# Optimization experiments

Measured on AMD Instinct MI355X. Metric: run time of the kernel, lower is better.

Reference implementation:

```python
import jax, jax.numpy as jnp
import numpy as np

N_NODES = 50000
N_FEAT = 128
N_HIDDEN = 256
N_CLASSES = 1
N_EDGES = 800000


def gcn_layer(x, src, dst, W, b, n_nodes):
    """GCNConv: D^-1/2 (A + I) D^-1/2 X W + b, via gather-scatter over edges."""
    h = x @ W  # [N, out]
    # add self loops
    loop = jnp.arange(n_nodes, dtype=src.dtype)
    s = jnp.concatenate([src, loop])
    d = jnp.concatenate([dst, loop])
    deg = jax.ops.segment_sum(jnp.ones_like(d, dtype=h.dtype), d, num_segments=n_nodes)
    inv_sqrt = jax.lax.rsqrt(jnp.maximum(deg, 1.0))
    norm = inv_sqrt[s] * inv_sqrt[d]  # [E+N]
    msgs = h[s] * norm[:, None]       # gather: [E+N, out]
    out = jax.ops.segment_sum(msgs, d, num_segments=n_nodes)  # scatter-add
    return out + b


def setup_inputs() -> dict:
    key = jax.random.key(0)
    k1, k2, k3, k4 = jax.random.split(key, 4)
    x = jax.random.normal(k1, (N_NODES, N_FEAT), dtype=jnp.float32)
    edge_index = jax.random.randint(k2, (2, N_EDGES), 0, N_NODES, dtype=jnp.int32)
    s1 = 1.0 / np.sqrt(N_FEAT)
    s2 = 1.0 / np.sqrt(N_HIDDEN)
    W1 = jax.random.uniform(k3, (N_FEAT, N_HIDDEN), jnp.float32, -s1, s1)
    b1 = jnp.zeros((N_HIDDEN,), jnp.float32)
    W2 = jax.random.uniform(k4, (N_HIDDEN, N_CLASSES), jnp.float32, -s2, s2)
    b2 = jnp.zeros((N_CLASSES,), jnp.float32)
    return {"x": x, "edge_index": edge_index, "W1": W1, "b1": b1, "W2": W2, "b2": b2}


def reference(x, edge_index, W1, b1, W2, b2):
    src, dst = edge_index[0], edge_index[1]
    n = x.shape[0]
    h = gcn_layer(x, src, dst, W1, b1, n)
    h = jax.nn.relu(h)  # dropout=0.0 -> identity
    out = gcn_layer(h, src, dst, W2, b2, n)
    return out  # [N, n_classes]
```

## Files before the change

kernel.cpp:

```cpp
#include <hip/hip_runtime.h>

typedef unsigned int uint;
typedef unsigned short ushort;
typedef __attribute__((ext_vector_type(8))) short short8;
typedef __attribute__((ext_vector_type(4))) float f32x4;

#define CAP   64
#define BM16  16
#define STR   68
#define NPB   192
#define NBIN  261
#define CAPB  4096
#define EPB   4096

__device__ __forceinline__ float bf_lo(uint p) { return __uint_as_float(p << 16); }
__device__ __forceinline__ float bf_hi(uint p) { return __uint_as_float(p & 0xffff0000u); }
__device__ __forceinline__ uint rne_lo(uint u) { return (u + 0x7fffu + ((u >> 16) & 1u)) >> 16; }
__device__ __forceinline__ uint rne_hi(uint u) { return (u + 0x7fffu + ((u >> 16) & 1u)) & 0xffff0000u; }

__global__ __launch_bounds__(1024) void k_part(
    const int* __restrict__ src, const int* __restrict__ dst,
    int* __restrict__ binCnt, uint* __restrict__ binData,
    const float* __restrict__ W1, uint* __restrict__ wpack, int E, int nblk_e) {
  int t = threadIdx.x;
  if ((int)blockIdx.x >= nblk_e) {
    int g = ((int)blockIdx.x - nblk_e) * 256 + (t & 255);
    if ((t >> 8) == 0 && g < 4096) {
      int kk = g >> 10, rem = g & 1023, ntile = rem >> 6, ln = rem & 63;
      int quad = ln >> 4, nn = ntile * 16 + (ln & 15);
      uint d[4];
#pragma unroll
      for (int jp = 0; jp < 4; ++jp) {
        int k = kk * 32 + quad * 8 + 2 * jp;
        uint lov = rne_lo(__float_as_uint(W1[k * 256 + nn]));
        uint hiv = rne_hi(__float_as_uint(W1[(k + 1) * 256 + nn]));
        d[jp] = lov | hiv;
      }
      *(uint4*)&wpack[g * 4] = make_uint4(d[0], d[1], d[2], d[3]);
    }
    return;
  }
  __shared__ int hist[NBIN];
  __shared__ int base[NBIN];
  for (int i = t; i < NBIN; i += 1024) hist[i] = 0;
  __syncthreads();
  int s[4], d[4], b[4];
  bool v[4];
#pragma unroll
  for (int j = 0; j < 4; ++j) {
    int e = blockIdx.x * EPB + j * 1024 + t;
    v[j] = e < E;
    if (v[j]) {
      s[j] = src[e];
      d[j] = dst[e];
      b[j] = d[j] / NPB;
      atomicAdd(&hist[b[j]], 1);
    }
  }
  __syncthreads();
  for (int i = t; i < NBIN; i += 1024) {
    int h = hist[i];
    base[i] = h ? atomicAdd(&binCnt[i], h) : 0;
    hist[i] = 0;
  }
  __syncthreads();
#pragma unroll
  for (int j = 0; j < 4; ++j) {
    if (v[j]) {
      int r = atomicAdd(&hist[b[j]], 1);
      int idx = base[b[j]] + r;
      if (idx < CAPB)
        binData[b[j] * CAPB + idx] = (uint)s[j] | ((uint)d[j] << 16);
    }
  }
}

__global__ __launch_bounds__(1024) void k_bucketize(
    const uint* __restrict__ binData, const int* __restrict__ binCnt,
    ushort* __restrict__ col, int* __restrict__ cnt,
    const float2* __restrict__ x2, uint* __restrict__ xs, float* __restrict__ inv,
    int N) {
  __shared__ ushort col_l[NPB * CAP];
  __shared__ int cnt_l[NPB];
  int b = blockIdx.x, t = threadIdx.x;
  int lo = b * NPB;
  for (int i = t; i < NPB; i += 1024) cnt_l[i] = 0;
  __syncthreads();
  int m = min(binCnt[b], CAPB);
  const uint* bd = &binData[b * CAPB];
  for (int e = t; e < m; e += 1024) {
    uint pr = bd[e];
    int sv = pr & 0xffffu;
    int dl = (int)(pr >> 16) - lo;
    int p = atomicAdd(&cnt_l[dl], 1);
    if (p < CAP) col_l[dl * CAP + p] = (ushort)sv;
  }
  __syncthreads();
  int nh = min(NPB, N - lo);
  if (nh <= 0) return;
  for (int i = t; i < nh; i += 1024) {
    int c = cnt_l[i];
    cnt[lo + i] = c;
    inv[lo + i] = rsqrtf((float)(c + 1));
  }
  uint* cg = (uint*)(col + (size_t)lo * CAP);
  const uint* cl = (const uint*)col_l;
  int nu = nh * (CAP / 2);
  for (int i = t; i < nu; i += 1024) cg[i] = cl[i];
  int nc = nh * 64;
  for (int i = t; i < nc; i += 1024) {
    int node = lo + (i >> 6);
    float invd = rsqrtf((float)(cnt_l[i >> 6] + 1));
    float2 f = x2[(size_t)node * 64 + (i & 63)];
    xs[(size_t)node * 64 + (i & 63)] =
        rne_lo(__float_as_uint(invd * f.x)) | rne_hi(__float_as_uint(invd * f.y));
  }
}

__global__ __launch_bounds__(256, 2) void k_agg_gemm(
    const uint* __restrict__ xs, const ushort* __restrict__ col,
    const int* __restrict__ cnt, const float* __restrict__ inv,
    const uint* __restrict__ wpack, const float* __restrict__ b1,
    const float* __restrict__ W2, float* __restrict__ cz, int N) {
  __shared__ uint As[BM16 * STR];
  __shared__ float red[64];
  int t = threadIdx.x, wave = t >> 6, lane = t & 63;
  int m0 = blockIdx.x * BM16;

  for (int rr = 0; rr < 4; ++rr) {
    int m = wave * 4 + rr;
    int node = m0 + m;
    float2 acc = make_float2(0.f, 0.f);
    if (node < N) {
      uint pd = xs[(size_t)node * 64 + lane];
      acc.x = bf_lo(pd);
      acc.y = bf_hi(pd);
      int e = min(cnt[node], CAP);
      int ce = (int)col[node * CAP + lane];
      int p = 0;
      for (; p + 15 < e; p += 16) {
        uint pv[16];
#pragma unroll
        for (int j = 0; j < 16; ++j) {
          int s = __shfl(ce, p + j);
          pv[j] = xs[(size_t)s * 64 + lane];
        }
#pragma unroll
        for (int j = 0; j < 16; ++j) { acc.x += bf_lo(pv[j]); acc.y += bf_hi(pv[j]); }
      }
      for (; p + 3 < e; p += 4) {
        uint pv[4];
#pragma unroll
        for (int j = 0; j < 4; ++j) {
          int s = __shfl(ce, p + j);
          pv[j] = xs[(size_t)s * 64 + lane];
        }
#pragma unroll
        for (int j = 0; j < 4; ++j) { acc.x += bf_lo(pv[j]); acc.y += bf_hi(pv[j]); }
      }
      for (; p < e; ++p) {
        int s = __shfl(ce, p);
        uint p0 = xs[(size_t)s * 64 + lane];
        acc.x += bf_lo(p0); acc.y += bf_hi(p0);
      }
      float invd = inv[node];
      acc.x *= invd;
      acc.y *= invd;
    }
    As[m * STR + lane] = rne_lo(__float_as_uint(acc.x)) | rne_hi(__float_as_uint(acc.y));
  }
  __syncthreads();

  int quad = lane >> 4, mrow = lane & 15;
  f32x4 acc[4];
#pragma unroll
  for (int nt = 0; nt < 4; ++nt) acc[nt] = (f32x4){0.f, 0.f, 0.f, 0.f};
#pragma unroll
  for (int kk = 0; kk < 4; ++kk) {
    short8 af = *(const short8*)&As[mrow * STR + kk * 16 + quad * 4];
#pragma unroll
    for (int nt = 0; nt < 4; ++nt) {
      int ntile = wave * 4 + nt;
      short8 bf = *(const short8*)&wpack[((kk * 16 + ntile) * 64 + lane) * 4];
      acc[nt] = __builtin_amdgcn_mfma_f32_16x16x32_bf16(af, bf, acc[nt], 0, 0, 0);
    }
  }

  float partial[4] = {0.f, 0.f, 0.f, 0.f};
#pragma unroll
  for (int nt = 0; nt < 4; ++nt) {
    int c = (wave * 4 + nt) * 16 + mrow;
    float b1c = b1[c], w2c = W2[c];
#pragma unroll
    for (int r = 0; r < 4; ++r) {
      float h = fmaxf(acc[nt][r] + b1c, 0.f);
      partial[r] = fmaf(h, w2c, partial[r]);
    }
  }
#pragma unroll
  for (int r = 0; r < 4; ++r) {
    float p = partial[r];
    p += __shfl_xor(p, 1); p += __shfl_xor(p, 2);
    p += __shfl_xor(p, 4); p += __shfl_xor(p, 8);
    if (mrow == 0) red[wave * 16 + quad * 4 + r] = p;
  }
  __syncthreads();
  if (t < 16) {
    int node = m0 + t;
    if (node < N) {
      float s = red[t] + red[16 + t] + red[32 + t] + red[48 + t];
      cz[node] = inv[node] * s;
    }
  }
}

__global__ void k_agg2(const ushort* __restrict__ col, const int* __restrict__ cnt,
                       const float* __restrict__ inv, const float* __restrict__ cz,
                       const float* __restrict__ b2, float* __restrict__ out, int N) {
  int g = blockIdx.x * blockDim.x + threadIdx.x;
  int node = g >> 2, q = g & 3;
  if (node >= N) return;
  int e = min(cnt[node], CAP);
  float acc = (q == 0) ? cz[node] : 0.f;
  const ushort* cp = &col[node * CAP];
  for (int p = q; p < e; p += 4) acc += cz[cp[p]];
  acc += __shfl_xor(acc, 1);
  acc += __shfl_xor(acc, 2);
  if (q == 0) out[node] = inv[node] * acc + b2[0];
}

extern "C" void kernel_launch(void* const* d_in, const int* in_sizes, int n_in,
                              void* d_out, int out_size, void* d_ws, size_t ws_size,
                              hipStream_t stream) {
  const float2* x2 = (const float2*)d_in[0];
  const int*    ei = (const int*)d_in[1];
  const float*  W1 = (const float*)d_in[2];
  const float*  b1 = (const float*)d_in[3];
  const float*  W2 = (const float*)d_in[4];
  const float*  b2 = (const float*)d_in[5];
  int N = in_sizes[0] / 128;
  int E = in_sizes[1] / 2;
  const int* src = ei;
  const int* dst = ei + E;
  float* out = (float*)d_out;

  char* w = (char*)d_ws;
  size_t o = 0;
  auto carve = [&](size_t bytes) { char* p = w + o; o += (bytes + 255) & ~(size_t)255; return p; };
  int*    binCnt  = (int*)   carve((size_t)NBIN * 4);
  int*    cnt     = (int*)   carve((size_t)N * 4);
  uint*   binData = (uint*)  carve((size_t)NBIN * CAPB * 4);
  ushort* col     = (ushort*)carve((size_t)N * CAP * 2);
  uint*   xs      = (uint*)  carve((size_t)N * 64 * 4);
  float*  inv     = (float*) carve((size_t)N * 4);
  uint*   wpack   = (uint*)  carve(16384 * 4);
  float*  cz      = (float*) carve((size_t)N * 4);

  hipMemsetAsync(binCnt, 0, (size_t)NBIN * sizeof(int), stream);

  int nblk_e = (E + EPB - 1) / EPB;
  k_part<<<nblk_e + 16, 1024, 0, stream>>>(src, dst, binCnt, binData, W1, wpack, E, nblk_e);

  k_bucketize<<<NBIN, 1024, 0, stream>>>(binData, binCnt, col, cnt, x2, xs, inv, N);

  k_agg_gemm<<<(N + BM16 - 1) / BM16, 256, 0, stream>>>(
      xs, col, cnt, inv, wpack, b1, W2, cz, N);

  long long tot2 = (long long)N * 4;
  k_agg2<<<(int)((tot2 + 255) / 256), 256, 0, stream>>>(col, cnt, inv, cz, b2, out, N);
}
```

Baseline: 147.3 us.

## Move bf16 conversion of x into partition kernel and apply source norms in aggregation

The fp32-to-bf16 conversion of node features moves out of the bucketize kernel and into extra blocks of the partition kernel, so it no longer waits on degree counts. Because the converted features are now unscaled, the aggregation kernel applies each source's 1/sqrt(deg) weight per edge via a shuffled coefficient and an FMA, and scales the self term by the node's own norm. This shortens the serial bucketize stage and overlaps the conversion with edge partitioning. The cost is a random read of cnt per neighbor, one rsqrt and one extra shuffle per edge in the gather loop, and slightly different bf16 rounding because scaling now happens after quantization.

```diff
diff --git a/kernel.cpp b/kernel.cpp
--- a/kernel.cpp
+++ b/kernel.cpp
@@ -12,6 +12,8 @@
 #define NBIN  261
 #define CAPB  4096
 #define EPB   4096
+#define NB_W  16
+#define NB_X  112
 
 __device__ __forceinline__ float bf_lo(uint p) { return __uint_as_float(p << 16); }
 __device__ __forceinline__ float bf_hi(uint p) { return __uint_as_float(p & 0xffff0000u); }
@@ -21,22 +23,33 @@
 __global__ __launch_bounds__(1024) void k_part(
     const int* __restrict__ src, const int* __restrict__ dst,
     int* __restrict__ binCnt, uint* __restrict__ binData,
-    const float* __restrict__ W1, uint* __restrict__ wpack, int E, int nblk_e) {
+    const float* __restrict__ W1, uint* __restrict__ wpack,
+    const float2* __restrict__ x2, uint* __restrict__ xs,
+    int E, int nconv, int nblk_e) {
   int t = threadIdx.x;
-  if ((int)blockIdx.x >= nblk_e) {
-    int g = ((int)blockIdx.x - nblk_e) * 256 + (t & 255);
-    if ((t >> 8) == 0 && g < 4096) {
-      int kk = g >> 10, rem = g & 1023, ntile = rem >> 6, ln = rem & 63;
-      int quad = ln >> 4, nn = ntile * 16 + (ln & 15);
-      uint d[4];
-#pragma unroll
-      for (int jp = 0; jp < 4; ++jp) {
-        int k = kk * 32 + quad * 8 + 2 * jp;
-        uint lov = rne_lo(__float_as_uint(W1[k * 256 + nn]));
-        uint hiv = rne_hi(__float_as_uint(W1[(k + 1) * 256 + nn]));
-        d[jp] = lov | hiv;
-      }
-      *(uint4*)&wpack[g * 4] = make_uint4(d[0], d[1], d[2], d[3]);
+  int bx = (int)blockIdx.x;
+  if (bx >= nblk_e) {
+    int role = bx - nblk_e;
+    if (role < NB_W) {
+      int g = role * 256 + (t & 255);
+      if ((t >> 8) == 0) {
+        int kk = g >> 10, rem = g & 1023, ntile = rem >> 6, ln = rem & 63;
+        int quad = ln >> 4, nn = ntile * 16 + (ln & 15);
+        uint d[4];
+#pragma unroll
+        for (int jp = 0; jp < 4; ++jp) {
+          int k = kk * 32 + quad * 8 + 2 * jp;
+          uint lov = rne_lo(__float_as_uint(W1[k * 256 + nn]));
+          uint hiv = rne_hi(__float_as_uint(W1[(k + 1) * 256 + nn]));
+          d[jp] = lov | hiv;
+        }
+        *(uint4*)&wpack[g * 4] = make_uint4(d[0], d[1], d[2], d[3]);
+      }
+    } else {
+      for (int g = (role - NB_W) * 1024 + t; g < nconv; g += NB_X * 1024) {
+        float2 f = x2[g];
+        xs[g] = rne_lo(__float_as_uint(f.x)) | rne_hi(__float_as_uint(f.y));
+      }
     }
     return;
   }
@@ -48,7 +61,7 @@
   bool v[4];
 #pragma unroll
   for (int j = 0; j < 4; ++j) {
-    int e = blockIdx.x * EPB + j * 1024 + t;
+    int e = bx * EPB + j * 1024 + t;
     v[j] = e < E;
     if (v[j]) {
       s[j] = src[e];
@@ -77,9 +90,7 @@
 
 __global__ __launch_bounds__(1024) void k_bucketize(
     const uint* __restrict__ binData, const int* __restrict__ binCnt,
-    ushort* __restrict__ col, int* __restrict__ cnt,
-    const float2* __restrict__ x2, uint* __restrict__ xs, float* __restrict__ inv,
-    int N) {
+    ushort* __restrict__ col, int* __restrict__ cnt, float* __restrict__ inv, int N) {
   __shared__ ushort col_l[NPB * CAP];
   __shared__ int cnt_l[NPB];
   int b = blockIdx.x, t = threadIdx.x;
@@ -107,14 +118,6 @@
   const uint* cl = (const uint*)col_l;
   int nu = nh * (CAP / 2);
   for (int i = t; i < nu; i += 1024) cg[i] = cl[i];
-  int nc = nh * 64;
-  for (int i = t; i < nc; i += 1024) {
-    int node = lo + (i >> 6);
-    float invd = rsqrtf((float)(cnt_l[i >> 6] + 1));
-    float2 f = x2[(size_t)node * 64 + (i & 63)];
-    xs[(size_t)node * 64 + (i & 63)] =
-        rne_lo(__float_as_uint(invd * f.x)) | rne_hi(__float_as_uint(invd * f.y));
-  }
 }
 
 __global__ __launch_bounds__(256, 2) void k_agg_gemm(
@@ -132,38 +135,49 @@
     int node = m0 + m;
     float2 acc = make_float2(0.f, 0.f);
     if (node < N) {
+      float invd = inv[node];
       uint pd = xs[(size_t)node * 64 + lane];
-      acc.x = bf_lo(pd);
-      acc.y = bf_hi(pd);
+      acc.x = invd * bf_lo(pd);
+      acc.y = invd * bf_hi(pd);
       int e = min(cnt[node], CAP);
       int ce = (int)col[node * CAP + lane];
+      float cw = rsqrtf((float)(cnt[ce] + 1));
       int p = 0;
       for (; p + 15 < e; p += 16) {
-        uint pv[16];
+        uint pv[16]; float cv[16];
 #pragma unroll
         for (int j = 0; j < 16; ++j) {
           int s = __shfl(ce, p + j);
+          cv[j] = __shfl(cw, p + j);
           pv[j] = xs[(size_t)s * 64 + lane];
         }
 #pragma unroll
-        for (int j = 0; j < 16; ++j) { acc.x += bf_lo(pv[j]); acc.y += bf_hi(pv[j]); }
+        for (int j = 0; j < 16; ++j) {
+          acc.x = fmaf(bf_lo(pv[j]), cv[j], acc.x);
+          acc.y = fmaf(bf_hi(pv[j]), cv[j], acc.y);
+        }
       }
       for (; p + 3 < e; p += 4) {
-        uint pv[4];
+        uint pv[4]; float cv[4];
 #pragma unroll
         for (int j = 0; j < 4; ++j) {
           int s = __shfl(ce, p + j);
+          cv[j] = __shfl(cw, p + j);
           pv[j] = xs[(size_t)s * 64 + lane];
         }
 #pragma unroll
-        for (int j = 0; j < 4; ++j) { acc.x += bf_lo(pv[j]); acc.y += bf_hi(pv[j]); }
+        for (int j = 0; j < 4; ++j) {
+          acc.x = fmaf(bf_lo(pv[j]), cv[j], acc.x);
+          acc.y = fmaf(bf_hi(pv[j]), cv[j], acc.y);
+        }
       }
       for (; p < e; ++p) {
         int s = __shfl(ce, p);
+        float c = __shfl(cw, p);
         uint p0 = xs[(size_t)s * 64 + lane];
-        acc.x += bf_lo(p0); acc.y += bf_hi(p0);
-      }
-      float invd = inv[node];
+        acc.x = fmaf(bf_lo(p0), c, acc.x);
+        acc.y = fmaf(bf_hi(p0), c, acc.y);
+      }
       acc.x *= invd;
       acc.y *= invd;
     }
@@ -258,10 +272,12 @@
 
   hipMemsetAsync(binCnt, 0, (size_t)NBIN * sizeof(int), stream);
 
+  int nconv = N * 64;
   int nblk_e = (E + EPB - 1) / EPB;
-  k_part<<<nblk_e + 16, 1024, 0, stream>>>(src, dst, binCnt, binData, W1, wpack, E, nblk_e);
-
-  k_bucketize<<<NBIN, 1024, 0, stream>>>(binData, binCnt, col, cnt, x2, xs, inv, N);
+  k_part<<<nblk_e + NB_W + NB_X, 1024, 0, stream>>>(
+      src, dst, binCnt, binData, W1, wpack, x2, xs, E, nconv, nblk_e);
+
+  k_bucketize<<<NBIN, 1024, 0, stream>>>(binData, binCnt, col, cnt, inv, N);
 
   k_agg_gemm<<<(N + BM16 - 1) / BM16, 256, 0, stream>>>(
       xs, col, cnt, inv, wpack, b1, W2, cz, N);
```

After: 149.8 us. Within noise of the previous version (+1.7%).

## Split x conversion into separate kernel and prefetch per-row metadata in aggregation

Applied to the files above, without the earlier changes.

Moves the scaling and bf16 packing of x out of the 261-block bucketize kernel into a new fully parallel elementwise kernel, so the conversion is no longer limited to a few large blocks. The aggregation kernel now loads count, column list, self feature and inverse degree for all four rows up front, so their latencies overlap. The cost is one extra launch and more registers held live in the aggregation kernel.

```diff
diff --git a/kernel.cpp b/kernel.cpp
--- a/kernel.cpp
+++ b/kernel.cpp
@@ -12,6 +12,7 @@
 #define NBIN  261
 #define CAPB  4096
 #define EPB   4096
+#define NB_W  16
 
 __device__ __forceinline__ float bf_lo(uint p) { return __uint_as_float(p << 16); }
 __device__ __forceinline__ float bf_hi(uint p) { return __uint_as_float(p & 0xffff0000u); }
@@ -23,9 +24,10 @@
     int* __restrict__ binCnt, uint* __restrict__ binData,
     const float* __restrict__ W1, uint* __restrict__ wpack, int E, int nblk_e) {
   int t = threadIdx.x;
-  if ((int)blockIdx.x >= nblk_e) {
-    int g = ((int)blockIdx.x - nblk_e) * 256 + (t & 255);
-    if ((t >> 8) == 0 && g < 4096) {
+  int bx = (int)blockIdx.x;
+  if (bx >= nblk_e) {
+    int g = (bx - nblk_e) * 256 + (t & 255);
+    if ((t >> 8) == 0) {
       int kk = g >> 10, rem = g & 1023, ntile = rem >> 6, ln = rem & 63;
       int quad = ln >> 4, nn = ntile * 16 + (ln & 15);
       uint d[4];
@@ -48,7 +50,7 @@
   bool v[4];
 #pragma unroll
   for (int j = 0; j < 4; ++j) {
-    int e = blockIdx.x * EPB + j * 1024 + t;
+    int e = bx * EPB + j * 1024 + t;
     v[j] = e < E;
     if (v[j]) {
       s[j] = src[e];
@@ -77,9 +79,7 @@
 
 __global__ __launch_bounds__(1024) void k_bucketize(
     const uint* __restrict__ binData, const int* __restrict__ binCnt,
-    ushort* __restrict__ col, int* __restrict__ cnt,
-    const float2* __restrict__ x2, uint* __restrict__ xs, float* __restrict__ inv,
-    int N) {
+    ushort* __restrict__ col, int* __restrict__ cnt, float* __restrict__ inv, int N) {
   __shared__ ushort col_l[NPB * CAP];
   __shared__ int cnt_l[NPB];
   int b = blockIdx.x, t = threadIdx.x;
@@ -107,13 +107,15 @@
   const uint* cl = (const uint*)col_l;
   int nu = nh * (CAP / 2);
   for (int i = t; i < nu; i += 1024) cg[i] = cl[i];
-  int nc = nh * 64;
-  for (int i = t; i < nc; i += 1024) {
-    int node = lo + (i >> 6);
-    float invd = rsqrtf((float)(cnt_l[i >> 6] + 1));
-    float2 f = x2[(size_t)node * 64 + (i & 63)];
-    xs[(size_t)node * 64 + (i & 63)] =
-        rne_lo(__float_as_uint(invd * f.x)) | rne_hi(__float_as_uint(invd * f.y));
+}
+
+__global__ void k_prep2(const float2* __restrict__ x2, const float* __restrict__ inv,
+                        uint* __restrict__ xs, int nconv) {
+  int gid = blockIdx.x * blockDim.x + threadIdx.x;
+  if (gid < nconv) {
+    float invd = inv[gid >> 6];
+    float2 f = x2[gid];
+    xs[gid] = rne_lo(__float_as_uint(invd * f.x)) | rne_hi(__float_as_uint(invd * f.y));
   }
 }
 
@@ -127,46 +129,51 @@
   int t = threadIdx.x, wave = t >> 6, lane = t & 63;
   int m0 = blockIdx.x * BM16;
 
+  int eA[4]; int ceA[4]; uint pdA[4]; float invA[4];
+#pragma unroll
+  for (int rr = 0; rr < 4; ++rr) {
+    int node = m0 + wave * 4 + rr;
+    bool ok = node < N;
+    int nc = ok ? node : 0;
+    eA[rr]   = ok ? min(cnt[nc], CAP) : 0;
+    ceA[rr]  = (int)col[(size_t)nc * CAP + lane];
+    pdA[rr]  = ok ? xs[(size_t)nc * 64 + lane] : 0u;
+    invA[rr] = ok ? inv[nc] : 0.f;
+  }
+
   for (int rr = 0; rr < 4; ++rr) {
     int m = wave * 4 + rr;
-    int node = m0 + m;
-    float2 acc = make_float2(0.f, 0.f);
-    if (node < N) {
-      uint pd = xs[(size_t)node * 64 + lane];
-      acc.x = bf_lo(pd);
-      acc.y = bf_hi(pd);
-      int e = min(cnt[node], CAP);
-      int ce = (int)col[node * CAP + lane];
-      int p = 0;
-      for (; p + 15 < e; p += 16) {
-        uint pv[16];
-#pragma unroll
-        for (int j = 0; j < 16; ++j) {
-          int s = __shfl(ce, p + j);
-          pv[j] = xs[(size_t)s * 64 + lane];
-        }
-#pragma unroll
-        for (int j = 0; j < 16; ++j) { acc.x += bf_lo(pv[j]); acc.y += bf_hi(pv[j]); }
+    float2 acc = make_float2(bf_lo(pdA[rr]), bf_hi(pdA[rr]));
+    int e = eA[rr];
+    int ce = ceA[rr];
+    int p = 0;
+    for (; p + 15 < e; p += 16) {
+      uint pv[16];
+#pragma unroll
+      for (int j = 0; j < 16; ++j) {
+        int s = __shfl(ce, p + j);
+        pv[j] = xs[(size_t)s * 64 + lane];
       }
-      for (; p + 3 < e; p += 4) {
-        uint pv[4];
-#pragma unroll
-        for (int j = 0; j < 4; ++j) {
-          int s = __shfl(ce, p + j);
-          pv[j] = xs[(size_t)s * 64 + lane];
-        }
-#pragma unroll
-        for (int j = 0; j < 4; ++j) { acc.x += bf_lo(pv[j]); acc.y += bf_hi(pv[j]); }
+#pragma unroll
+      for (int j = 0; j < 16; ++j) { acc.x += bf_lo(pv[j]); acc.y += bf_hi(pv[j]); }
+    }
+    for (; p + 3 < e; p += 4) {
+      uint pv[4];
+#pragma unroll
+      for (int j = 0; j < 4; ++j) {
+        int s = __shfl(ce, p + j);
+        pv[j] = xs[(size_t)s * 64 + lane];
       }
-      for (; p < e; ++p) {
-        int s = __shfl(ce, p);
-        uint p0 = xs[(size_t)s * 64 + lane];
-        acc.x += bf_lo(p0); acc.y += bf_hi(p0);
-      }
-      float invd = inv[node];
-      acc.x *= invd;
-      acc.y *= invd;
-    }
+#pragma unroll
+      for (int j = 0; j < 4; ++j) { acc.x += bf_lo(pv[j]); acc.y += bf_hi(pv[j]); }
+    }
+    for (; p < e; ++p) {
+      int s = __shfl(ce, p);
+      uint p0 = xs[(size_t)s * 64 + lane];
+      acc.x += bf_lo(p0); acc.y += bf_hi(p0);
+    }
+    acc.x *= invA[rr];
+    acc.y *= invA[rr];
     As[m * STR + lane] = rne_lo(__float_as_uint(acc.x)) | rne_hi(__float_as_uint(acc.y));
   }
   __syncthreads();
@@ -259,9 +266,12 @@
   hipMemsetAsync(binCnt, 0, (size_t)NBIN * sizeof(int), stream);
 
   int nblk_e = (E + EPB - 1) / EPB;
-  k_part<<<nblk_e + 16, 1024, 0, stream>>>(src, dst, binCnt, binData, W1, wpack, E, nblk_e);
-
-  k_bucketize<<<NBIN, 1024, 0, stream>>>(binData, binCnt, col, cnt, x2, xs, inv, N);
+  k_part<<<nblk_e + NB_W, 1024, 0, stream>>>(src, dst, binCnt, binData, W1, wpack, E, nblk_e);
+
+  k_bucketize<<<NBIN, 1024, 0, stream>>>(binData, binCnt, col, cnt, inv, N);
+
+  int nconv = N * 64;
+  k_prep2<<<(nconv + 255) / 256, 256, 0, stream>>>(x2, inv, xs, nconv);
 
   k_agg_gemm<<<(N + BM16 - 1) / BM16, 256, 0, stream>>>(
       xs, col, cnt, inv, wpack, b1, W2, cz, N);
```

Result: no change. 148.0 us (+0.4%).
